# Performance work log

Hardware: AMD Instinct MI355X
Metric: run time of the kernel (lower is better)

Reference implementation:

```python
import jax, jax.numpy as jnp
import numpy as np

HIDDEN = 1024
HEADS = 16
HEAD_SIZE = HIDDEN // HEADS
N, L = 2, 2048


def setup_inputs() -> dict:
    key = jax.random.key(0)
    ks = jax.random.split(key, 9)
    s = 1.0 / np.sqrt(HIDDEN)
    x = jax.random.normal(ks[0], (N, L, HIDDEN), dtype=jnp.float32)
    Wq = jax.random.normal(ks[1], (HIDDEN, HIDDEN), dtype=jnp.float32) * s
    Wk = jax.random.normal(ks[2], (HIDDEN, HIDDEN), dtype=jnp.float32) * s
    Wv = jax.random.normal(ks[3], (HIDDEN, HIDDEN), dtype=jnp.float32) * s
    Wo = jax.random.normal(ks[4], (HIDDEN, HIDDEN), dtype=jnp.float32) * s
    bq = jax.random.normal(ks[5], (HIDDEN,), dtype=jnp.float32) * s
    bk = jax.random.normal(ks[6], (HIDDEN,), dtype=jnp.float32) * s
    bv = jax.random.normal(ks[7], (HIDDEN,), dtype=jnp.float32) * s
    bo = jax.random.normal(ks[8], (HIDDEN,), dtype=jnp.float32) * s
    return {"x": x, "Wq": Wq, "bq": bq, "Wk": Wk, "bk": bk,
            "Wv": Wv, "bv": bv, "Wo": Wo, "bo": bo}


def reference(x, Wq, bq, Wk, bk, Wv, bv, Wo, bo):
    n, l, _ = x.shape
    # torch Linear: y = x @ W.T + b
    q = (x @ Wq.T + bq).reshape(n, l, HEADS, HEAD_SIZE)
    k = (x @ Wk.T + bk).reshape(n, l, HEADS, HEAD_SIZE)
    v = (x @ Wv.T + bv).reshape(n, l, HEADS, HEAD_SIZE)
    # NOTE: module does NOT apply 1/sqrt(head_size) scaling
    sims = jnp.einsum('nqhs,nkhs->nhqk', q, k)  # (N,H,L,L)
    attn = jax.nn.softmax(sims, axis=-1)
    ctx = jnp.einsum('nhqk,nkhs->nqhs', attn, v).reshape(n, l, HIDDEN)
    return ctx @ Wo.T + bo
```

## Files before the change

### kernel.cpp

```cpp
#include <hip/hip_runtime.h>
#include <hip/hip_bf16.h>
#include <stdint.h>
#include <stddef.h>

#define HIDDEN 1024
#define HEADS  16
#define HDIM   64
#define NBATCH 2
#define SEQ    2048
#define TOK    (NBATCH*SEQ)

typedef __attribute__((ext_vector_type(8))) short bf16x8;
typedef __attribute__((ext_vector_type(4))) float f32x4;
typedef unsigned short bf16u;

__device__ __forceinline__ unsigned short f2bf(float f) {
  union { float f; unsigned int u; } c; c.f = f;
  unsigned int u = c.u;
  unsigned int r = (u + 0x7fffu + ((u >> 16) & 1u)) >> 16;
  return (unsigned short)r;
}

__device__ __forceinline__ unsigned int pk2bf(float a, float b) {
  __hip_bfloat16 ba = __float2bfloat16(a), bb = __float2bfloat16(b);
  unsigned short ua, ub;
  __builtin_memcpy(&ua, &ba, 2);
  __builtin_memcpy(&ub, &bb, 2);
  return (unsigned int)ua | ((unsigned int)ub << 16);
}

__global__ __launch_bounds__(256) void convert_kernel(
    const float* __restrict__ x,
    const float* __restrict__ wq, const float* __restrict__ wk,
    const float* __restrict__ wv, const float* __restrict__ wo,
    bf16u* __restrict__ xb, bf16u* __restrict__ wqkvb, bf16u* __restrict__ wob) {
  const int XG = TOK*HIDDEN/4;
  const int WG = HIDDEN*HIDDEN/4;
  int i = blockIdx.x*blockDim.x + threadIdx.x;
  const float* src; bf16u* dst; int off;
  if (i < XG)            { src = x;  dst = xb;                      off = i; }
  else if (i < XG+WG)    { src = wq; dst = wqkvb;                   off = i-XG; }
  else if (i < XG+2*WG)  { src = wk; dst = wqkvb +   HIDDEN*HIDDEN; off = i-XG-WG; }
  else if (i < XG+3*WG)  { src = wv; dst = wqkvb + 2*HIDDEN*HIDDEN; off = i-XG-2*WG; }
  else if (i < XG+4*WG)  { src = wo; dst = wob;                     off = i-XG-3*WG; }
  else return;
  float4 v = ((const float4*)src)[off];
  ushort4 o;
  o.x = f2bf(v.x); o.y = f2bf(v.y); o.z = f2bf(v.z); o.w = f2bf(v.w);
  *(ushort4*)&dst[(size_t)off*4] = o;
}

__device__ __forceinline__ void gemm_core(const bf16u* __restrict__ Abase,
                                          const bf16u* __restrict__ Bbase,
                                          bf16u* As, bf16u* Bs,
                                          f32x4 (&acc)[4][4]) {
  const int K = HIDDEN;
  const int t = threadIdx.x;
  const int w = t >> 6, lane = t & 63;
  const int wm = (w >> 1) * 64, wn = (w & 1) * 64;
  const int row = lane & 15, kq = (lane >> 4) * 8;
  const int c0 = t, c1 = t + 256;
  const int rA0 = c0 >> 2, k80 = (c0 & 3) * 8;
  const int rA1 = c1 >> 2, k81 = (c1 & 3) * 8;
  bf16u* ldsA0 = As + (size_t)(w*64)*8;
  bf16u* ldsA1 = As + (size_t)(256 + w*64)*8;
  bf16u* ldsB0 = Bs + (size_t)(w*64)*8;
  bf16u* ldsB1 = Bs + (size_t)(256 + w*64)*8;

  for (int k0 = 0; k0 < K; k0 += 32) {
    __builtin_amdgcn_global_load_lds(
        (const __attribute__((address_space(1))) void*)(Abase + (size_t)rA0*K + k0 + k80),
        (__attribute__((address_space(3))) void*)ldsA0, 16, 0, 0);
    __builtin_amdgcn_global_load_lds(
        (const __attribute__((address_space(1))) void*)(Abase + (size_t)rA1*K + k0 + k81),
        (__attribute__((address_space(3))) void*)ldsA1, 16, 0, 0);
    __builtin_amdgcn_global_load_lds(
        (const __attribute__((address_space(1))) void*)(Bbase + (size_t)rA0*K + k0 + k80),
        (__attribute__((address_space(3))) void*)ldsB0, 16, 0, 0);
    __builtin_amdgcn_global_load_lds(
        (const __attribute__((address_space(1))) void*)(Bbase + (size_t)rA1*K + k0 + k81),
        (__attribute__((address_space(3))) void*)ldsB1, 16, 0, 0);
    __syncthreads();
    bf16x8 af[4], bf[4];
    #pragma unroll
    for (int mi = 0; mi < 4; mi++)
      af[mi] = *(const bf16x8*)&As[(wm + mi*16 + row)*32 + kq];
    #pragma unroll
    for (int ni = 0; ni < 4; ni++)
      bf[ni] = *(const bf16x8*)&Bs[(wn + ni*16 + row)*32 + kq];
    #pragma unroll
    for (int mi = 0; mi < 4; mi++)
      #pragma unroll
      for (int ni = 0; ni < 4; ni++)
        acc[mi][ni] = __builtin_amdgcn_mfma_f32_16x16x32_bf16(af[mi], bf[ni], acc[mi][ni], 0, 0, 0);
    __syncthreads();
  }
}

__global__ __launch_bounds__(256) void qkv_kernel(
    const bf16u* __restrict__ xb, const bf16u* __restrict__ wqkvb,
    const float* __restrict__ bq, const float* __restrict__ bk, const float* __restrict__ bv,
    bf16u* __restrict__ qb, bf16u* __restrict__ kb, bf16u* __restrict__ vtb) {
  __shared__ bf16u As[128*32];
  __shared__ bf16u Bs[128*32];
  f32x4 z = {0.f,0.f,0.f,0.f};
  f32x4 acc[4][4];
  #pragma unroll
  for (int i = 0; i < 4; i++)
    #pragma unroll
    for (int j = 0; j < 4; j++) acc[i][j] = z;
  const int n0 = blockIdx.x * 128, m0 = blockIdx.y * 128;
  gemm_core(xb + (size_t)m0*HIDDEN, wqkvb + (size_t)n0*HIDDEN, As, Bs, acc);

  const int t = threadIdx.x, w = t >> 6, lane = t & 63;
  const int wm = (w >> 1) * 64, wn = (w & 1) * 64;
  #pragma unroll
  for (int mi = 0; mi < 4; mi++) {
    #pragma unroll
    for (int ni = 0; ni < 4; ni++) {
      const int col = n0 + wn + ni*16 + (lane & 15);
      const int which = col >> 10, c = col & 1023;
      const int head = c >> 6, d = c & 63;
      const float bias = (which == 0 ? bq : (which == 1 ? bk : bv))[c];
      #pragma unroll
      for (int j = 0; j < 4; j++) {
        const int rowm = m0 + wm + mi*16 + ((lane >> 4) * 4) + j;
        const int n = rowm >> 11, l = rowm & 2047;
        const bf16u hv = f2bf(acc[mi][ni][j] + bias);
        if (which == 0)
          qb[(((size_t)n*HEADS + head)*SEQ + l)*HDIM + d] = hv;
        else if (which == 1)
          kb[(((size_t)n*HEADS + head)*SEQ + l)*HDIM + d] = hv;
        else
          vtb[(((size_t)n*HEADS + head)*HDIM + d)*SEQ + l] = hv;
      }
    }
  }
}

__global__ __launch_bounds__(256) void attn_kernel(
    const bf16u* __restrict__ qb, const bf16u* __restrict__ kb,
    const bf16u* __restrict__ vtb, bf16u* __restrict__ ctxb) {
  __shared__ bf16u Ks[2][64*64];
  __shared__ bf16u Vs[2][64*64];
  __shared__ bf16u Pl[4][16*64];
  const int t = threadIdx.x, w = t >> 6, lane = t & 63;
  const int row = lane & 15, hi = lane >> 4, kq8 = hi * 8;
  const int qt = blockIdx.x, nh = blockIdx.y;
  const int n = nh >> 4, h = nh & 15;
  const bf16u* Qb = qb  + (size_t)nh * SEQ * HDIM;
  const bf16u* Kb = kb  + (size_t)nh * SEQ * HDIM;
  const bf16u* Vt = vtb + (size_t)nh * HDIM * SEQ;

  const int c0 = w*64 + lane, c1 = c0 + 256;
  const int r0 = c0 >> 3, e0 = ((c0 & 7) ^ (r0 & 7)) * 8;
  const int r1 = c1 >> 3, e1 = ((c1 & 7) ^ (r1 & 7)) * 8;

  const int qrow = qt*64 + w*16 + row;
  const bf16x8 aq0 = *(const bf16x8*)&Qb[(size_t)qrow*HDIM + kq8];
  const bf16x8 aq1 = *(const bf16x8*)&Qb[(size_t)qrow*HDIM + 32 + kq8];
  const short one_bf = (short)0x3F80;
  const bf16x8 vone = {one_bf, one_bf, one_bf, one_bf, one_bf, one_bf, one_bf, one_bf};
  f32x4 z = {0.f,0.f,0.f,0.f};
  float mr = -1e30f;
  f32x4 ao[4] = {z,z,z,z};
  f32x4 aden = z;
  bf16u* P = &Pl[w][0];

  auto stage = [&](int buf, int kv0) {
    __builtin_amdgcn_global_load_lds(
        (const __attribute__((address_space(1))) void*)(Kb + (size_t)(kv0 + r0)*HDIM + e0),
        (__attribute__((address_space(3))) void*)(&Ks[buf][(size_t)(w*64)*8]), 16, 0, 0);
    __builtin_amdgcn_global_load_lds(
        (const __attribute__((address_space(1))) void*)(Kb + (size_t)(kv0 + r1)*HDIM + e1),
        (__attribute__((address_space(3))) void*)(&Ks[buf][(size_t)(256 + w*64)*8]), 16, 0, 0);
    __builtin_amdgcn_global_load_lds(
        (const __attribute__((address_space(1))) void*)(Vt + (size_t)r0*SEQ + kv0 + e0),
        (__attribute__((address_space(3))) void*)(&Vs[buf][(size_t)(w*64)*8]), 16, 0, 0);
    __builtin_amdgcn_global_load_lds(
        (const __attribute__((address_space(1))) void*)(Vt + (size_t)r1*SEQ + kv0 + e1),
        (__attribute__((address_space(3))) void*)(&Vs[buf][(size_t)(256 + w*64)*8]), 16, 0, 0);
  };

  stage(0, 0);
  asm volatile("s_waitcnt vmcnt(0)" ::: "memory");
  __builtin_amdgcn_s_barrier();

  for (int it = 0; it < 32; ++it) {
    const int cur = it & 1;
    if (it < 31) stage(cur ^ 1, (it + 1) * 64);

    f32x4 s[4];
    bf16x8 bk0[4], bk1[4];
    #pragma unroll
    for (int cb = 0; cb < 4; cb++) {
      const int kvr = cb*16 + row;
      const int sw = kvr & 7;
      bk0[cb] = *(const bf16x8*)&Ks[cur][kvr*64 + ((hi     ^ sw) * 8)];
      bk1[cb] = *(const bf16x8*)&Ks[cur][kvr*64 + (((4+hi) ^ sw) * 8)];
    }
    __builtin_amdgcn_s_setprio(1);
    #pragma unroll
    for (int cb = 0; cb < 4; cb++) {
      s[cb] = __builtin_amdgcn_mfma_f32_16x16x32_bf16(bk0[cb], aq0, z, 0, 0, 0);
      s[cb] = __builtin_amdgcn_mfma_f32_16x16x32_bf16(bk1[cb], aq1, s[cb], 0, 0, 0);
    }
    __builtin_amdgcn_s_setprio(0);

    float pm = s[0][0];
    #pragma unroll
    for (int cb = 0; cb < 4; cb++)
      #pragma unroll
      for (int j = 0; j < 4; j++)
        pm = fmaxf(pm, s[cb][j]);
    pm = fmaxf(pm, __shfl_xor(pm, 16));
    pm = fmaxf(pm, __shfl_xor(pm, 32));

    if (!__all(pm <= mr)) {
      const float nm = fmaxf(mr, pm);
      const float sc = __expf(mr - nm);
      mr = nm;
      float scj[4];
      #pragma unroll
      for (int j = 0; j < 4; j++)
        scj[j] = __shfl(sc, hi*4 + j);
      #pragma unroll
      for (int j = 0; j < 4; j++)
        aden[j] *= scj[j];
      #pragma unroll
      for (int db = 0; db < 4; db++)
        #pragma unroll
        for (int j = 0; j < 4; j++)
          ao[db][j] *= scj[j];
    }

    float p[4][4];
    #pragma unroll
    for (int cb = 0; cb < 4; cb++)
      #pragma unroll
      for (int j = 0; j < 4; j++)
        p[cb][j] = __expf(s[cb][j] - mr);

    #pragma unroll
    for (int cb = 0; cb < 4; cb++) {
      uint2 pk;
      pk.x = pk2bf(p[cb][0], p[cb][1]);
      pk.y = pk2bf(p[cb][2], p[cb][3]);
      const int slot = cb*2 + (hi >> 1);
      *(uint2*)&P[row*64 + ((slot ^ (row & 7)) * 8) + (hi & 1)*4] = pk;
    }
    asm volatile("s_waitcnt lgkmcnt(0)" ::: "memory");
    __builtin_amdgcn_sched_barrier(0);

    bf16x8 ap[2], bv[2][4];
    #pragma unroll
    for (int ks = 0; ks < 2; ks++) {
      ap[ks] = *(const bf16x8*)&P[row*64 + (((ks*4+hi) ^ (row & 7)) * 8)];
      #pragma unroll
      for (int db = 0; db < 4; db++) {
        const int dr = db*16 + row;
        bv[ks][db] = *(const bf16x8*)&Vs[cur][dr*64 + (((ks*4+hi) ^ (dr & 7)) * 8)];
      }
    }
    __builtin_amdgcn_s_setprio(1);
    #pragma unroll
    for (int ks = 0; ks < 2; ks++) {
      #pragma unroll
      for (int db = 0; db < 4; db++)
        ao[db] = __builtin_amdgcn_mfma_f32_16x16x32_bf16(ap[ks], bv[ks][db], ao[db], 0, 0, 0);
      aden = __builtin_amdgcn_mfma_f32_16x16x32_bf16(ap[ks], vone, aden, 0, 0, 0);
    }
    __builtin_amdgcn_s_setprio(0);

    if (it < 31) asm volatile("s_waitcnt vmcnt(0)" ::: "memory");
    __builtin_amdgcn_s_barrier();
  }

  float invj[4];
  #pragma unroll
  for (int j = 0; j < 4; j++)
    invj[j] = 1.0f / aden[j];
  #pragma unroll
  for (int db = 0; db < 4; db++)
    #pragma unroll
    for (int j = 0; j < 4; j++) {
      const int l = qt*64 + w*16 + hi*4 + j;
      const int d = db*16 + row;
      ctxb[((size_t)n*SEQ + l)*HIDDEN + h*HDIM + d] = f2bf(ao[db][j] * invj[j]);
    }
}

__global__ __launch_bounds__(256) void oproj_kernel(
    const bf16u* __restrict__ ctxb, const bf16u* __restrict__ wob,
    const float* __restrict__ bo, float* __restrict__ out) {
  __shared__ bf16u As[128*32];
  __shared__ bf16u Bs[128*32];
  f32x4 z = {0.f,0.f,0.f,0.f};
  f32x4 acc[4][4];
  #pragma unroll
  for (int i = 0; i < 4; i++)
    #pragma unroll
    for (int j = 0; j < 4; j++) acc[i][j] = z;
  const int n0 = blockIdx.x * 128, m0 = blockIdx.y * 128;
  gemm_core(ctxb + (size_t)m0*HIDDEN, wob + (size_t)n0*HIDDEN, As, Bs, acc);

  const int t = threadIdx.x, w = t >> 6, lane = t & 63;
  const int wm = (w >> 1) * 64, wn = (w & 1) * 64;
  #pragma unroll
  for (int mi = 0; mi < 4; mi++) {
    #pragma unroll
    for (int ni = 0; ni < 4; ni++) {
      const int col = n0 + wn + ni*16 + (lane & 15);
      const float bias = bo[col];
      #pragma unroll
      for (int j = 0; j < 4; j++) {
        const int rowm = m0 + wm + mi*16 + ((lane >> 4)*4) + j;
        out[(size_t)rowm*HIDDEN + col] = acc[mi][ni][j] + bias;
      }
    }
  }
}

extern "C" void kernel_launch(void* const* d_in, const int* in_sizes, int n_in,
                              void* d_out, int out_size, void* d_ws, size_t ws_size,
                              hipStream_t stream) {
  const float* x  = (const float*)d_in[0];
  const float* Wq = (const float*)d_in[1];
  const float* bq = (const float*)d_in[2];
  const float* Wk = (const float*)d_in[3];
  const float* bk = (const float*)d_in[4];
  const float* Wv = (const float*)d_in[5];
  const float* bv = (const float*)d_in[6];
  const float* Wo = (const float*)d_in[7];
  const float* bo = (const float*)d_in[8];
  float* out = (float*)d_out;

  bf16u* xb    = (bf16u*)d_ws;
  bf16u* wqkvb = xb    + (size_t)TOK*HIDDEN;
  bf16u* wob   = wqkvb + (size_t)3*HIDDEN*HIDDEN;
  bf16u* qb    = wob   + (size_t)HIDDEN*HIDDEN;
  bf16u* kb    = qb    + (size_t)TOK*HIDDEN;
  bf16u* vtb   = kb    + (size_t)TOK*HIDDEN;
  bf16u* ctxb  = vtb   + (size_t)TOK*HIDDEN;

  convert_kernel<<<8192, 256, 0, stream>>>(x, Wq, Wk, Wv, Wo, xb, wqkvb, wob);
  qkv_kernel<<<dim3(24, 32), 256, 0, stream>>>(xb, wqkvb, bq, bk, bv, qb, kb, vtb);
  attn_kernel<<<dim3(32, 32), 256, 0, stream>>>(qb, kb, vtb, ctxb);
  oproj_kernel<<<dim3(8, 32), 256, 0, stream>>>(ctxb, wob, bo, out);
}
```

Measured before the change: 240.7 us.

## Process 32 query rows per wave in attention to reuse K/V tiles

Each wave now handles two 16-row query sub-tiles (128 queries per block), so every K and V fragment loaded from LDS feeds twice as many MFMAs. The grid shrinks from 32x32 to 16x32 blocks, halving global K/V staging traffic per query. The cost is more registers for the doubled accumulators, softmax state and P buffer, plus fewer blocks (512) to fill the GPU's compute units.

```diff
diff --git a/kernel.cpp b/kernel.cpp
--- a/kernel.cpp
+++ b/kernel.cpp
@@ -143,9 +143,9 @@
     const bf16u* __restrict__ vtb, bf16u* __restrict__ ctxb) {
   __shared__ bf16u Ks[2][64*64];
   __shared__ bf16u Vs[2][64*64];
-  __shared__ bf16u Pl[4][16*64];
+  __shared__ bf16u Pl[4][32*64];
   const int t = threadIdx.x, w = t >> 6, lane = t & 63;
-  const int row = lane & 15, hi = lane >> 4, kq8 = hi * 8;
+  const int row = lane & 15, hi = lane >> 4;
   const int qt = blockIdx.x, nh = blockIdx.y;
   const int n = nh >> 4, h = nh & 15;
   const bf16u* Qb = qb  + (size_t)nh * SEQ * HDIM;
@@ -156,15 +156,20 @@
   const int r0 = c0 >> 3, e0 = ((c0 & 7) ^ (r0 & 7)) * 8;
   const int r1 = c1 >> 3, e1 = ((c1 & 7) ^ (r1 & 7)) * 8;
 
-  const int qrow = qt*64 + w*16 + row;
-  const bf16x8 aq0 = *(const bf16x8*)&Qb[(size_t)qrow*HDIM + kq8];
-  const bf16x8 aq1 = *(const bf16x8*)&Qb[(size_t)qrow*HDIM + 32 + kq8];
+  const int qbase = qt*128 + w*32;
+  bf16x8 aq[2][2];
+  #pragma unroll
+  for (int qh = 0; qh < 2; qh++)
+    #pragma unroll
+    for (int kc = 0; kc < 2; kc++)
+      aq[qh][kc] = *(const bf16x8*)&Qb[(size_t)(qbase + qh*16 + row)*HDIM + kc*32 + hi*8];
+
   const short one_bf = (short)0x3F80;
   const bf16x8 vone = {one_bf, one_bf, one_bf, one_bf, one_bf, one_bf, one_bf, one_bf};
   f32x4 z = {0.f,0.f,0.f,0.f};
-  float mr = -1e30f;
-  f32x4 ao[4] = {z,z,z,z};
-  f32x4 aden = z;
+  float mr[2] = {-1e30f, -1e30f};
+  f32x4 ao[2][4] = {{z,z,z,z},{z,z,z,z}};
+  f32x4 aden[2] = {z, z};
   bf16u* P = &Pl[w][0];
 
   auto stage = [&](int buf, int kv0) {
@@ -190,7 +195,7 @@
     const int cur = it & 1;
     if (it < 31) stage(cur ^ 1, (it + 1) * 64);
 
-    f32x4 s[4];
+    f32x4 s[4][2];
     bf16x8 bk0[4], bk1[4];
     #pragma unroll
     for (int cb = 0; cb < 4; cb++) {
@@ -201,74 +206,87 @@
     }
     __builtin_amdgcn_s_setprio(1);
     #pragma unroll
-    for (int cb = 0; cb < 4; cb++) {
-      s[cb] = __builtin_amdgcn_mfma_f32_16x16x32_bf16(bk0[cb], aq0, z, 0, 0, 0);
-      s[cb] = __builtin_amdgcn_mfma_f32_16x16x32_bf16(bk1[cb], aq1, s[cb], 0, 0, 0);
-    }
+    for (int cb = 0; cb < 4; cb++)
+      #pragma unroll
+      for (int qh = 0; qh < 2; qh++) {
+        s[cb][qh] = __builtin_amdgcn_mfma_f32_16x16x32_bf16(bk0[cb], aq[qh][0], z, 0, 0, 0);
+        s[cb][qh] = __builtin_amdgcn_mfma_f32_16x16x32_bf16(bk1[cb], aq[qh][1], s[cb][qh], 0, 0, 0);
+      }
     __builtin_amdgcn_s_setprio(0);
 
-    float pm = s[0][0];
-    #pragma unroll
-    for (int cb = 0; cb < 4; cb++)
-      #pragma unroll
-      for (int j = 0; j < 4; j++)
-        pm = fmaxf(pm, s[cb][j]);
-    pm = fmaxf(pm, __shfl_xor(pm, 16));
-    pm = fmaxf(pm, __shfl_xor(pm, 32));
-
-    if (!__all(pm <= mr)) {
-      const float nm = fmaxf(mr, pm);
-      const float sc = __expf(mr - nm);
-      mr = nm;
-      float scj[4];
-      #pragma unroll
-      for (int j = 0; j < 4; j++)
-        scj[j] = __shfl(sc, hi*4 + j);
-      #pragma unroll
-      for (int j = 0; j < 4; j++)
-        aden[j] *= scj[j];
-      #pragma unroll
-      for (int db = 0; db < 4; db++)
+    float pm[2];
+    #pragma unroll
+    for (int qh = 0; qh < 2; qh++) {
+      float m0 = s[0][qh][0];
+      #pragma unroll
+      for (int cb = 0; cb < 4; cb++)
         #pragma unroll
         for (int j = 0; j < 4; j++)
-          ao[db][j] *= scj[j];
-    }
-
-    float p[4][4];
-    #pragma unroll
-    for (int cb = 0; cb < 4; cb++)
-      #pragma unroll
-      for (int j = 0; j < 4; j++)
-        p[cb][j] = __expf(s[cb][j] - mr);
-
-    #pragma unroll
-    for (int cb = 0; cb < 4; cb++) {
-      uint2 pk;
-      pk.x = pk2bf(p[cb][0], p[cb][1]);
-      pk.y = pk2bf(p[cb][2], p[cb][3]);
-      const int slot = cb*2 + (hi >> 1);
-      *(uint2*)&P[row*64 + ((slot ^ (row & 7)) * 8) + (hi & 1)*4] = pk;
+          m0 = fmaxf(m0, s[cb][qh][j]);
+      m0 = fmaxf(m0, __shfl_xor(m0, 16));
+      m0 = fmaxf(m0, __shfl_xor(m0, 32));
+      pm[qh] = m0;
+    }
+
+    if (__any((pm[0] > mr[0]) || (pm[1] > mr[1]))) {
+      #pragma unroll
+      for (int qh = 0; qh < 2; qh++) {
+        const float nm = fmaxf(mr[qh], pm[qh]);
+        const float sc = __expf(mr[qh] - nm);
+        mr[qh] = nm;
+        float scj[4];
+        #pragma unroll
+        for (int j = 0; j < 4; j++)
+          scj[j] = __shfl(sc, hi*4 + j);
+        #pragma unroll
+        for (int j = 0; j < 4; j++)
+          aden[qh][j] *= scj[j];
+        #pragma unroll
+        for (int db = 0; db < 4; db++)
+          #pragma unroll
+          for (int j = 0; j < 4; j++)
+            ao[qh][db][j] *= scj[j];
+      }
+    }
+
+    #pragma unroll
+    for (int qh = 0; qh < 2; qh++) {
+      const int pr = qh*16 + row;
+      #pragma unroll
+      for (int cb = 0; cb < 4; cb++) {
+        uint2 pk;
+        pk.x = pk2bf(__expf(s[cb][qh][0] - mr[qh]), __expf(s[cb][qh][1] - mr[qh]));
+        pk.y = pk2bf(__expf(s[cb][qh][2] - mr[qh]), __expf(s[cb][qh][3] - mr[qh]));
+        const int slot = cb*2 + (hi >> 1);
+        *(uint2*)&P[pr*64 + ((slot ^ (row & 7)) * 8) + (hi & 1)*4] = pk;
+      }
     }
     asm volatile("s_waitcnt lgkmcnt(0)" ::: "memory");
     __builtin_amdgcn_sched_barrier(0);
 
-    bf16x8 ap[2], bv[2][4];
-    #pragma unroll
-    for (int ks = 0; ks < 2; ks++) {
-      ap[ks] = *(const bf16x8*)&P[row*64 + (((ks*4+hi) ^ (row & 7)) * 8)];
+    bf16x8 ap[2][2], bv[2][4];
+    #pragma unroll
+    for (int qh = 0; qh < 2; qh++)
+      #pragma unroll
+      for (int ks = 0; ks < 2; ks++)
+        ap[qh][ks] = *(const bf16x8*)&P[(qh*16 + row)*64 + (((ks*4+hi) ^ (row & 7)) * 8)];
+    #pragma unroll
+    for (int ks = 0; ks < 2; ks++)
       #pragma unroll
       for (int db = 0; db < 4; db++) {
         const int dr = db*16 + row;
         bv[ks][db] = *(const bf16x8*)&Vs[cur][dr*64 + (((ks*4+hi) ^ (dr & 7)) * 8)];
       }
-    }
     __builtin_amdgcn_s_setprio(1);
     #pragma unroll
     for (int ks = 0; ks < 2; ks++) {
       #pragma unroll
-      for (int db = 0; db < 4; db++)
-        ao[db] = __builtin_amdgcn_mfma_f32_16x16x32_bf16(ap[ks], bv[ks][db], ao[db], 0, 0, 0);
-      aden = __builtin_amdgcn_mfma_f32_16x16x32_bf16(ap[ks], vone, aden, 0, 0, 0);
+      for (int qh = 0; qh < 2; qh++) {
+        #pragma unroll
+        for (int db = 0; db < 4; db++)
+          ao[qh][db] = __builtin_amdgcn_mfma_f32_16x16x32_bf16(ap[qh][ks], bv[ks][db], ao[qh][db], 0, 0, 0);
+        aden[qh] = __builtin_amdgcn_mfma_f32_16x16x32_bf16(ap[qh][ks], vone, aden[qh], 0, 0, 0);
+      }
     }
     __builtin_amdgcn_s_setprio(0);
 
@@ -276,18 +294,21 @@
     __builtin_amdgcn_s_barrier();
   }
 
-  float invj[4];
-  #pragma unroll
-  for (int j = 0; j < 4; j++)
-    invj[j] = 1.0f / aden[j];
-  #pragma unroll
-  for (int db = 0; db < 4; db++)
-    #pragma unroll
-    for (int j = 0; j < 4; j++) {
-      const int l = qt*64 + w*16 + hi*4 + j;
-      const int d = db*16 + row;
-      ctxb[((size_t)n*SEQ + l)*HIDDEN + h*HDIM + d] = f2bf(ao[db][j] * invj[j]);
-    }
+  #pragma unroll
+  for (int qh = 0; qh < 2; qh++) {
+    float invj[4];
+    #pragma unroll
+    for (int j = 0; j < 4; j++)
+      invj[j] = 1.0f / aden[qh][j];
+    #pragma unroll
+    for (int db = 0; db < 4; db++)
+      #pragma unroll
+      for (int j = 0; j < 4; j++) {
+        const int l = qt*128 + w*32 + qh*16 + hi*4 + j;
+        const int d = db*16 + row;
+        ctxb[((size_t)n*SEQ + l)*HIDDEN + h*HDIM + d] = f2bf(ao[qh][db][j] * invj[j]);
+      }
+  }
 }
 
 __global__ __launch_bounds__(256) void oproj_kernel(
@@ -345,6 +366,6 @@
 
   convert_kernel<<<8192, 256, 0, stream>>>(x, Wq, Wk, Wv, Wo, xb, wqkvb, wob);
   qkv_kernel<<<dim3(24, 32), 256, 0, stream>>>(xb, wqkvb, bq, bk, bv, qb, kb, vtb);
-  attn_kernel<<<dim3(32, 32), 256, 0, stream>>>(qb, kb, vtb, ctxb);
+  attn_kernel<<<dim3(16, 32), 256, 0, stream>>>(qb, kb, vtb, ctxb);
   oproj_kernel<<<dim3(8, 32), 256, 0, stream>>>(ctxb, wob, bo, out);
 }
```

After: 228.6 us. -5.0%, faster.
